# Performance work log

Measured on AMD Instinct MI355X. Metric: run time of the kernel, lower is better.

## Reference

```python
import jax, jax.numpy as jnp
import numpy as np

B = 262144
IN = 12
HID = 256
OUT = 12


def setup_inputs() -> dict:
    key = jax.random.key(0)
    ks = jax.random.split(key, 7)
    def lin(k, fan_in, fan_out):
        kw, kb = jax.random.split(k)
        bound = 1.0 / np.sqrt(fan_in)
        W = jax.random.uniform(kw, (fan_in, fan_out), jnp.float32, -bound, bound)
        b = jax.random.uniform(kb, (fan_out,), jnp.float32, -bound, bound)
        return W, b
    W1, b1 = lin(ks[0], IN, HID)
    W2, b2 = lin(ks[1], HID, HID)
    W3, b3 = lin(ks[2], HID, OUT)
    inp = jax.random.normal(ks[3], (B, IN), jnp.float32)
    return {"inp": inp, "W1": W1, "b1": b1, "W2": W2, "b2": b2, "W3": W3, "b3": b3}


def _forward(inp, W1, b1, W2, b2, W3, b3):
    h = jax.nn.relu(inp @ W1 + b1)
    h = jax.nn.relu(h @ W2 + b2)
    x = h @ W3 + b3  # [B, 12]

    pos = jnp.tanh(x[:, 0:3])
    vel = jnp.tanh(x[:, 3:6])
    pts = jax.nn.sigmoid(x[:, 6:7])
    clus = jnp.tanh(x[:, 7:10])
    sun = jnp.tanh(x[:, 10:12])

    # position clipped to unit sphere
    dist = jnp.linalg.norm(pos, axis=1, keepdims=True)  # [B,1]
    pos_c = jnp.where(dist > 1.0, pos / dist, pos)

    # inspected points: over-estimates set to 1, under-estimates set to previous
    prev = inp[:, 6:7]
    pts_c = jnp.where(pts > 1.0, 1.0, pts)
    pts_c = jnp.where(pts < prev, prev, pts_c)

    # cluster: push away from deputy if moving toward it, then clip to unit sphere
    delta = clus - inp[:, 7:10]
    deputy = inp[:, 0:3] - inp[:, 7:10]
    nd = deputy / jnp.linalg.norm(deputy, axis=1, keepdims=True)
    dd = jnp.einsum('ij,ij->i', delta, deputy)[:, None]  # [B,1]
    offset = jnp.where(dd > 0.0, clus - nd, clus)
    cdist = jnp.linalg.norm(offset, axis=1, keepdims=True)
    # NOTE: non-exceeding rows keep the ORIGINAL tanh prediction (torch semantics)
    clus_c = jnp.where(cdist > 1.0, offset / cdist, clus)

    # sun angle projected onto unit circle
    sun_c = sun / jnp.linalg.norm(sun, axis=1, keepdims=True)

    return jnp.concatenate([pos_c, vel, pts_c, clus_c, sun_c], axis=1)


def reference(inp, W1, b1, W2, b2, W3, b3):
    return _forward(inp, W1, b1, W2, b2, W3, b3)
```

## Files before the change

kernel.cpp:

```cpp
#include <hip/hip_runtime.h>
#include <math.h>

#define NIN 12
#define HID 256
#define NOUT 12
#define BM 64
#define NBLK (262144 / BM)

typedef _Float16 f16;
typedef f16 f16x8 __attribute__((ext_vector_type(8)));
typedef float f32x4 __attribute__((ext_vector_type(4)));

__device__ __forceinline__ void gll16(const void* g, void* l) {
    __builtin_amdgcn_global_load_lds(
        (const __attribute__((address_space(1))) unsigned int*)g,
        (__attribute__((address_space(3))) unsigned int*)l, 16, 0, 0);
}

__global__ void prep_w2(const float* __restrict__ W2, f16* __restrict__ w2p) {
    const int e = (blockIdx.x * 256 + threadIdx.x) * 4;
    const int k = e >> 8, col0 = e & 255;
    const float4 w = *(const float4*)(W2 + k * HID + col0);
    const int s = k >> 5, lgw = (k >> 3) & 3, j = k & 7;
    #pragma unroll
    for (int q = 0; q < 4; ++q) {
        const float v = ((const float*)&w)[q];
        const f16 hi = (f16)v;
        const f16 lo = (f16)(v - (float)hi);
        const int c = col0 + q, ct = c >> 4, cc = c & 15, l = (lgw << 4) | cc;
        w2p[(size_t)(((s*2 + 0)*16 + ct)*64 + l)*8 + j] = hi;
        w2p[(size_t)(((s*2 + 1)*16 + ct)*64 + l)*8 + j] = lo;
    }
}

__global__ __launch_bounds__(256, 3)
void mlp_main(const float* __restrict__ inp, const float* __restrict__ W1,
              const float* __restrict__ b1, const float* __restrict__ W2,
              const float* __restrict__ b2, const float* __restrict__ W3,
              const float* __restrict__ b3, const f16* __restrict__ w2p,
              float* __restrict__ out)
{
    __shared__ __align__(16) unsigned char smem[48896];
    __shared__ int nflag;
    __shared__ int flaglist[16];

    f16*   Bl   = (f16*)smem;
    float* W3s  = (float*)(smem + 32768);
    float* b2s  = (float*)(smem + 45056);
    float* h1f  = (float*)(smem + 46080);
    float* h2f  = (float*)(smem + 47104);
    float* psum = (float*)(smem + 48128);

    const int t    = threadIdx.x;
    const int lane = t & 63;
    const int wid  = t >> 6;
    const int cl   = lane & 15;
    const int lg   = lane >> 4;
    const int row0 = blockIdx.x * BM;

    if (t == 0) nflag = 0;

    {
        const char* w3c = (const char*)W3;
        #pragma unroll
        for (int i = 0; i < 3; ++i) {
            const int off = (wid*3 + i) * 1024;
            gll16(w3c + off + lane*16, (char*)W3s + off);
        }
        if (wid == 0) gll16((const char*)b2 + lane*16, (char*)b2s);
    }

    const int myrow = row0 + wid*16 + cl;
    float xin[12];
    {
        const f32x4* ip = (const f32x4*)(inp + (size_t)myrow * NIN);
        const f32x4 a = ip[0], b = ip[1], c = ip[2];
        xin[0]=a.x; xin[1]=a.y; xin[2]=a.z; xin[3]=a.w;
        xin[4]=b.x; xin[5]=b.y; xin[6]=b.z; xin[7]=b.w;
        xin[8]=c.x; xin[9]=c.y; xin[10]=c.z; xin[11]=c.w;
    }

    f32x4 acc[16];
    {
        const f32x4 zero = {0.f, 0.f, 0.f, 0.f};
        #pragma unroll
        for (int ct = 0; ct < 16; ++ct) acc[ct] = zero;
    }
    for (int s = 0; s < 8; ++s) {
        __syncthreads();
        const char* src = (const char*)w2p + (size_t)s * 32768;
        #pragma unroll
        for (int i = 0; i < 8; ++i) {
            const int off = (i*4 + wid) * 1024;
            gll16(src + off + lane*16, (char*)Bl + off);
        }
        const int k0 = 32*s + 8*lg;
        float a0[8];
        {
            const f32x4 bb0 = *(const f32x4*)(b1 + k0);
            const f32x4 bb1 = *(const f32x4*)(b1 + k0 + 4);
            a0[0]=bb0.x; a0[1]=bb0.y; a0[2]=bb0.z; a0[3]=bb0.w;
            a0[4]=bb1.x; a0[5]=bb1.y; a0[6]=bb1.z; a0[7]=bb1.w;
        }
        #pragma unroll
        for (int m = 0; m < 12; ++m) {
            const float xm = xin[m];
            const f32x4 w0 = *(const f32x4*)(W1 + m*HID + k0);
            const f32x4 w1 = *(const f32x4*)(W1 + m*HID + k0 + 4);
            a0[0] = fmaf(xm, w0.x, a0[0]); a0[1] = fmaf(xm, w0.y, a0[1]);
            a0[2] = fmaf(xm, w0.z, a0[2]); a0[3] = fmaf(xm, w0.w, a0[3]);
            a0[4] = fmaf(xm, w1.x, a0[4]); a0[5] = fmaf(xm, w1.y, a0[5]);
            a0[6] = fmaf(xm, w1.z, a0[6]); a0[7] = fmaf(xm, w1.w, a0[7]);
        }
        f16x8 ahi, alo;
        #pragma unroll
        for (int j = 0; j < 8; ++j) {
            const float h = fmaxf(a0[j], 0.f);
            const f16 hi = (f16)h;
            ahi[j] = hi;
            alo[j] = (f16)(h - (float)hi);
        }
        asm volatile("s_waitcnt vmcnt(0)" ::: "memory");
        __syncthreads();
        #pragma unroll
        for (int ct = 0; ct < 16; ++ct) {
            const f16x8 bhi = *(const f16x8*)((const char*)Bl + (size_t)(( 0 + ct)*64 + lane)*16);
            const f16x8 blo = *(const f16x8*)((const char*)Bl + (size_t)((16 + ct)*64 + lane)*16);
            acc[ct] = __builtin_amdgcn_mfma_f32_16x16x32_f16(ahi, bhi, acc[ct], 0, 0, 0);
            acc[ct] = __builtin_amdgcn_mfma_f32_16x16x32_f16(ahi, blo, acc[ct], 0, 0, 0);
            acc[ct] = __builtin_amdgcn_mfma_f32_16x16x32_f16(alo, bhi, acc[ct], 0, 0, 0);
        }
    }

    float part[4][12];
    #pragma unroll
    for (int q = 0; q < 4; ++q)
        #pragma unroll
        for (int jj = 0; jj < 12; ++jj) part[q][jj] = 0.f;

    #pragma unroll
    for (int ct = 0; ct < 16; ++ct) {
        const int col = ct*16 + cl;
        const float bv = b2s[col];
        const f32x4 w3a = *(const f32x4*)(W3s + col*12);
        const f32x4 w3b = *(const f32x4*)(W3s + col*12 + 4);
        const f32x4 w3c = *(const f32x4*)(W3s + col*12 + 8);
        #pragma unroll
        for (int q = 0; q < 4; ++q) {
            const float h2 = fmaxf(acc[ct][q] + bv, 0.f);
            part[q][0]  = fmaf(h2, w3a.x, part[q][0]);
            part[q][1]  = fmaf(h2, w3a.y, part[q][1]);
            part[q][2]  = fmaf(h2, w3a.z, part[q][2]);
            part[q][3]  = fmaf(h2, w3a.w, part[q][3]);
            part[q][4]  = fmaf(h2, w3b.x, part[q][4]);
            part[q][5]  = fmaf(h2, w3b.y, part[q][5]);
            part[q][6]  = fmaf(h2, w3b.z, part[q][6]);
            part[q][7]  = fmaf(h2, w3b.w, part[q][7]);
            part[q][8]  = fmaf(h2, w3c.x, part[q][8]);
            part[q][9]  = fmaf(h2, w3c.y, part[q][9]);
            part[q][10] = fmaf(h2, w3c.z, part[q][10]);
            part[q][11] = fmaf(h2, w3c.w, part[q][11]);
        }
    }
    #pragma unroll
    for (int m = 1; m < 16; m <<= 1) {
        #pragma unroll
        for (int q = 0; q < 4; ++q)
            #pragma unroll
            for (int jj = 0; jj < 12; ++jj)
                part[q][jj] += __shfl_xor(part[q][jj], m);
    }

    if (cl < 4) {
        const int q = cl;
        const int R = wid*16 + 4*lg + q;
        const int grow = row0 + R;
        float x[12];
        #pragma unroll
        for (int jj = 0; jj < 12; ++jj) x[jj] = part[q][jj] + b3[jj];

        const f32x4* ip = (const f32x4*)(inp + (size_t)grow * NIN);
        const f32x4 iA = ip[0], iB = ip[1], iC = ip[2];
        const float in0=iA.x, in1=iA.y, in2=iA.z, in6=iB.z, in7=iB.w, in8=iC.x, in9=iC.y;

        const float pos0=tanhf(x[0]), pos1=tanhf(x[1]), pos2=tanhf(x[2]);
        const float vel0=tanhf(x[3]), vel1=tanhf(x[4]), vel2=tanhf(x[5]);
        const float pts = 1.f/(1.f+expf(-x[6]));
        const float cl0=tanhf(x[7]), cl1=tanhf(x[8]), cl2=tanhf(x[9]);
        const float sn0=tanhf(x[10]), sn1=tanhf(x[11]);

        const float dist = sqrtf(pos0*pos0 + pos1*pos1 + pos2*pos2);
        float pc0=pos0, pc1=pos1, pc2=pos2;
        if (dist > 1.0f) { pc0 = pos0/dist; pc1 = pos1/dist; pc2 = pos2/dist; }

        const float prev = in6;
        float pts_c = (pts > 1.0f) ? 1.0f : pts;
        pts_c = (pts < prev) ? prev : pts_c;

        const float de0 = cl0-in7, de1 = cl1-in8, de2 = cl2-in9;
        const float dp0 = in0-in7, dp1 = in1-in8, dp2 = in2-in9;
        const float dpn = sqrtf(dp0*dp0 + dp1*dp1 + dp2*dp2);
        const float nd0 = dp0/dpn, nd1 = dp1/dpn, nd2 = dp2/dpn;
        const float dd  = de0*dp0 + de1*dp1 + de2*dp2;
        float off0, off1, off2;
        if (dd > 0.0f) { off0 = cl0-nd0; off1 = cl1-nd1; off2 = cl2-nd2; }
        else           { off0 = cl0;     off1 = cl1;     off2 = cl2;     }
        const float cdist = sqrtf(off0*off0 + off1*off1 + off2*off2);
        float cc0, cc1, cc2;
        if (cdist > 1.0f) { cc0 = off0/cdist; cc1 = off1/cdist; cc2 = off2/cdist; }
        else              { cc0 = cl0;        cc1 = cl1;        cc2 = cl2;        }

        const float snn = sqrtf(sn0*sn0 + sn1*sn1);
        const float sc0 = sn0/snn, sc1 = sn1/snn;

        if (fabsf(dd) < 2e-4f || (dd > 0.f && fabsf(cdist - 1.f) < 2e-4f)) {
            const int slot = atomicAdd(&nflag, 1);
            if (slot < 16) flaglist[slot] = R;
        }

        f32x4* dst = (f32x4*)(out + (size_t)grow * NOUT);
        f32x4 o0 = {pc0, pc1, pc2, vel0};
        f32x4 o1 = {vel1, vel2, pts_c, cc0};
        f32x4 o2 = {cc1, cc2, sc0, sc1};
        dst[0] = o0; dst[1] = o1; dst[2] = o2;
    }
    __syncthreads();

    const int nf = (nflag < 16) ? nflag : 16;
    for (int f = 0; f < nf; ++f) {
        const int grow = row0 + flaglist[f];
        {
            float a = b1[t];
            const float* xr = inp + (size_t)grow * NIN;
            #pragma unroll
            for (int m = 0; m < 12; ++m) a = fmaf(xr[m], W1[m*HID + t], a);
            h1f[t] = fmaxf(a, 0.f);
        }
        __syncthreads();
        {
            float a = b2[t];
            for (int k = 0; k < HID; ++k) a = fmaf(h1f[k], W2[k*HID + t], a);
            h2f[t] = fmaxf(a, 0.f);
        }
        __syncthreads();
        if (t < 12*16) {
            const int jj = t >> 4, seg = t & 15;
            float a = 0.f;
            #pragma unroll
            for (int u = 0; u < 16; ++u) a = fmaf(h2f[seg*16 + u], W3[(seg*16 + u)*NOUT + jj], a);
            psum[jj*16 + seg] = a;
        }
        __syncthreads();
        if (t == 0) {
            float x[12];
            #pragma unroll
            for (int jj = 0; jj < 12; ++jj) {
                float sacc = b3[jj];
                for (int g = 0; g < 16; ++g) sacc += psum[jj*16 + g];
                x[jj] = sacc;
            }
            const float* xr = inp + (size_t)grow * NIN;
            const float in0=xr[0], in1=xr[1], in2=xr[2], in6=xr[6], in7=xr[7], in8=xr[8], in9=xr[9];
            const float pos0=tanhf(x[0]), pos1=tanhf(x[1]), pos2=tanhf(x[2]);
            const float vel0=tanhf(x[3]), vel1=tanhf(x[4]), vel2=tanhf(x[5]);
            const float pts = 1.f/(1.f+expf(-x[6]));
            const float cl0=tanhf(x[7]), cl1=tanhf(x[8]), cl2=tanhf(x[9]);
            const float sn0=tanhf(x[10]), sn1=tanhf(x[11]);
            const float dist = sqrtf(pos0*pos0 + pos1*pos1 + pos2*pos2);
            float pc0=pos0, pc1=pos1, pc2=pos2;
            if (dist > 1.0f) { pc0 = pos0/dist; pc1 = pos1/dist; pc2 = pos2/dist; }
            const float prev = in6;
            float pts_c = (pts > 1.0f) ? 1.0f : pts;
            pts_c = (pts < prev) ? prev : pts_c;
            const float de0 = cl0-in7, de1 = cl1-in8, de2 = cl2-in9;
            const float dp0 = in0-in7, dp1 = in1-in8, dp2 = in2-in9;
            const float dpn = sqrtf(dp0*dp0 + dp1*dp1 + dp2*dp2);
            const float nd0 = dp0/dpn, nd1 = dp1/dpn, nd2 = dp2/dpn;
            const float dd  = de0*dp0 + de1*dp1 + de2*dp2;
            float off0, off1, off2;
            if (dd > 0.0f) { off0 = cl0-nd0; off1 = cl1-nd1; off2 = cl2-nd2; }
            else           { off0 = cl0;     off1 = cl1;     off2 = cl2;     }
            const float cdist = sqrtf(off0*off0 + off1*off1 + off2*off2);
            float cc0, cc1, cc2;
            if (cdist > 1.0f) { cc0 = off0/cdist; cc1 = off1/cdist; cc2 = off2/cdist; }
            else              { cc0 = cl0;        cc1 = cl1;        cc2 = cl2;        }
            const float snn = sqrtf(sn0*sn0 + sn1*sn1);
            const float sc0 = sn0/snn, sc1 = sn1/snn;
            float* dst = out + (size_t)grow * NOUT;
            dst[0]=pc0; dst[1]=pc1; dst[2]=pc2; dst[3]=vel0; dst[4]=vel1; dst[5]=vel2;
            dst[6]=pts_c; dst[7]=cc0; dst[8]=cc1; dst[9]=cc2; dst[10]=sc0; dst[11]=sc1;
        }
        __syncthreads();
    }
}

extern "C" void kernel_launch(void* const* d_in, const int* in_sizes, int n_in,
                              void* d_out, int out_size, void* d_ws, size_t ws_size,
                              hipStream_t stream) {
    const float* inp = (const float*)d_in[0];
    const float* W1  = (const float*)d_in[1];
    const float* b1  = (const float*)d_in[2];
    const float* W2  = (const float*)d_in[3];
    const float* b2  = (const float*)d_in[4];
    const float* W3  = (const float*)d_in[5];
    const float* b3  = (const float*)d_in[6];
    float* out = (float*)d_out;
    f16* w2p = (f16*)d_ws;

    hipLaunchKernelGGL(prep_w2, dim3(64), dim3(256), 0, stream, W2, w2p);
    hipLaunchKernelGGL(mlp_main, dim3(NBLK), dim3(256), 0, stream,
                       inp, W1, b1, W2, b2, W3, b3, (const f16*)w2p, out);
}
```

Before: 269.6 us.

## Split hidden columns across two wave groups with 512-thread blocks

Doubles the block to 512 threads. Each group of four waves now computes half of the 256 hidden-layer-2 columns, so each wave holds 8 accumulator tiles instead of 16. The partial layer-3 sums from the two halves go into shared memory and are combined by 64 threads before the epilogue. This cuts per-wave register pressure and allows more waves in flight per CU. The cost is that the layer-1 activations are computed twice, plus an extra shared-memory round trip and barrier.

```diff
diff --git a/kernel.cpp b/kernel.cpp
--- a/kernel.cpp
+++ b/kernel.cpp
@@ -5,6 +5,7 @@
 #define HID 256
 #define NOUT 12
 #define BM 64
+#define THREADS 512
 #define NBLK (262144 / BM)
 
 typedef _Float16 f16;
@@ -33,27 +34,29 @@
     }
 }
 
-__global__ __launch_bounds__(256, 3)
+__global__ __launch_bounds__(THREADS, 4)
 void mlp_main(const float* __restrict__ inp, const float* __restrict__ W1,
               const float* __restrict__ b1, const float* __restrict__ W2,
               const float* __restrict__ b2, const float* __restrict__ W3,
               const float* __restrict__ b3, const f16* __restrict__ w2p,
               float* __restrict__ out)
 {
-    __shared__ __align__(16) unsigned char smem[48896];
+    __shared__ __align__(16) unsigned char smem[54272];
     __shared__ int nflag;
     __shared__ int flaglist[16];
 
     f16*   Bl   = (f16*)smem;
     float* W3s  = (float*)(smem + 32768);
     float* b2s  = (float*)(smem + 45056);
-    float* h1f  = (float*)(smem + 46080);
-    float* h2f  = (float*)(smem + 47104);
-    float* psum = (float*)(smem + 48128);
+    float* psum = (float*)(smem + 46080);
+    float* h1f  = (float*)(smem + 52224);
+    float* h2f  = (float*)(smem + 53248);
 
     const int t    = threadIdx.x;
     const int lane = t & 63;
     const int wid  = t >> 6;
+    const int wr   = wid & 3;
+    const int wc   = wid >> 2;
     const int cl   = lane & 15;
     const int lg   = lane >> 4;
     const int row0 = blockIdx.x * BM;
@@ -62,15 +65,12 @@
 
     {
         const char* w3c = (const char*)W3;
-        #pragma unroll
-        for (int i = 0; i < 3; ++i) {
-            const int off = (wid*3 + i) * 1024;
-            gll16(w3c + off + lane*16, (char*)W3s + off);
-        }
-        if (wid == 0) gll16((const char*)b2 + lane*16, (char*)b2s);
-    }
-
-    const int myrow = row0 + wid*16 + cl;
+        gll16(w3c + wid * 1024 + lane * 16, (char*)W3s + wid * 1024);
+        if (wid < 4) gll16(w3c + (8 + wid) * 1024 + lane * 16, (char*)W3s + (8 + wid) * 1024);
+        if (wid == 4) gll16((const char*)b2 + lane * 16, (char*)b2s);
+    }
+
+    const int myrow = row0 + wr * 16 + cl;
     float xin[12];
     {
         const f32x4* ip = (const f32x4*)(inp + (size_t)myrow * NIN);
@@ -80,21 +80,21 @@
         xin[8]=c.x; xin[9]=c.y; xin[10]=c.z; xin[11]=c.w;
     }
 
-    f32x4 acc[16];
+    f32x4 acc[8];
     {
         const f32x4 zero = {0.f, 0.f, 0.f, 0.f};
         #pragma unroll
-        for (int ct = 0; ct < 16; ++ct) acc[ct] = zero;
+        for (int ct = 0; ct < 8; ++ct) acc[ct] = zero;
     }
     for (int s = 0; s < 8; ++s) {
         __syncthreads();
         const char* src = (const char*)w2p + (size_t)s * 32768;
         #pragma unroll
-        for (int i = 0; i < 8; ++i) {
-            const int off = (i*4 + wid) * 1024;
-            gll16(src + off + lane*16, (char*)Bl + off);
-        }
-        const int k0 = 32*s + 8*lg;
+        for (int i = 0; i < 4; ++i) {
+            const int off = (i * 8 + wid) * 1024;
+            gll16(src + off + lane * 16, (char*)Bl + off);
+        }
+        const int k0 = 32 * s + 8 * lg;
         float a0[8];
         {
             const f32x4 bb0 = *(const f32x4*)(b1 + k0);
@@ -123,9 +123,10 @@
         asm volatile("s_waitcnt vmcnt(0)" ::: "memory");
         __syncthreads();
         #pragma unroll
-        for (int ct = 0; ct < 16; ++ct) {
-            const f16x8 bhi = *(const f16x8*)((const char*)Bl + (size_t)(( 0 + ct)*64 + lane)*16);
-            const f16x8 blo = *(const f16x8*)((const char*)Bl + (size_t)((16 + ct)*64 + lane)*16);
+        for (int ct = 0; ct < 8; ++ct) {
+            const int gct = wc * 8 + ct;
+            const f16x8 bhi = *(const f16x8*)((const char*)Bl + (size_t)(( 0 + gct)*64 + lane)*16);
+            const f16x8 blo = *(const f16x8*)((const char*)Bl + (size_t)((16 + gct)*64 + lane)*16);
             acc[ct] = __builtin_amdgcn_mfma_f32_16x16x32_f16(ahi, bhi, acc[ct], 0, 0, 0);
             acc[ct] = __builtin_amdgcn_mfma_f32_16x16x32_f16(ahi, blo, acc[ct], 0, 0, 0);
             acc[ct] = __builtin_amdgcn_mfma_f32_16x16x32_f16(alo, bhi, acc[ct], 0, 0, 0);
@@ -139,8 +140,8 @@
         for (int jj = 0; jj < 12; ++jj) part[q][jj] = 0.f;
 
     #pragma unroll
-    for (int ct = 0; ct < 16; ++ct) {
-        const int col = ct*16 + cl;
+    for (int ct = 0; ct < 8; ++ct) {
+        const int col = (wc * 8 + ct) * 16 + cl;
         const float bv = b2s[col];
         const f32x4 w3a = *(const f32x4*)(W3s + col*12);
         const f32x4 w3b = *(const f32x4*)(W3s + col*12 + 4);
@@ -170,14 +171,21 @@
             for (int jj = 0; jj < 12; ++jj)
                 part[q][jj] += __shfl_xor(part[q][jj], m);
     }
-
     if (cl < 4) {
-        const int q = cl;
-        const int R = wid*16 + 4*lg + q;
-        const int grow = row0 + R;
+        const int R = wr * 16 + 4 * lg + cl;
+        float* p = psum + (size_t)(wc * BM + R) * 12;
+        #pragma unroll
+        for (int jj = 0; jj < 12; ++jj) p[jj] = part[cl][jj];
+    }
+    __syncthreads();
+
+    if (t < BM) {
+        const int r = t;
+        const int grow = row0 + r;
         float x[12];
         #pragma unroll
-        for (int jj = 0; jj < 12; ++jj) x[jj] = part[q][jj] + b3[jj];
+        for (int jj = 0; jj < 12; ++jj)
+            x[jj] = psum[r * 12 + jj] + psum[(BM + r) * 12 + jj] + b3[jj];
 
         const f32x4* ip = (const f32x4*)(inp + (size_t)grow * NIN);
         const f32x4 iA = ip[0], iB = ip[1], iC = ip[2];
@@ -215,7 +223,7 @@
 
         if (fabsf(dd) < 2e-4f || (dd > 0.f && fabsf(cdist - 1.f) < 2e-4f)) {
             const int slot = atomicAdd(&nflag, 1);
-            if (slot < 16) flaglist[slot] = R;
+            if (slot < 16) flaglist[slot] = r;
         }
 
         f32x4* dst = (f32x4*)(out + (size_t)grow * NOUT);
@@ -229,7 +237,7 @@
     const int nf = (nflag < 16) ? nflag : 16;
     for (int f = 0; f < nf; ++f) {
         const int grow = row0 + flaglist[f];
-        {
+        if (t < HID) {
             float a = b1[t];
             const float* xr = inp + (size_t)grow * NIN;
             #pragma unroll
@@ -237,7 +245,7 @@
             h1f[t] = fmaxf(a, 0.f);
         }
         __syncthreads();
-        {
+        if (t < HID) {
             float a = b2[t];
             for (int k = 0; k < HID; ++k) a = fmaf(h1f[k], W2[k*HID + t], a);
             h2f[t] = fmaxf(a, 0.f);
@@ -308,6 +316,6 @@
     f16* w2p = (f16*)d_ws;
 
     hipLaunchKernelGGL(prep_w2, dim3(64), dim3(256), 0, stream, W2, w2p);
-    hipLaunchKernelGGL(mlp_main, dim3(NBLK), dim3(256), 0, stream,
+    hipLaunchKernelGGL(mlp_main, dim3(NBLK), dim3(THREADS), 0, stream,
                        inp, W1, b1, W2, b2, W3, b3, (const f16*)w2p, out);
 }
```

Result: slower. 448.9 us (+66.5%).
